# Kernel tuning notes

Measured on AMD Instinct MI355X. Metric: run time of the kernel, lower is better.

## Reference

```python
import jax, jax.numpy as jnp
import numpy as np

EPS = 1e-5

def conv1x1(x, w):
    # x: [B,C,H,W], w: [O,C] -> [B,O,H,W]
    return jnp.einsum('oc,bchw->bohw', w, x)

def bn(x, g, b, m, v):
    # inference batchnorm over channel dim 1
    scale = g / jnp.sqrt(v + EPS)
    return x * scale[None, :, None, None] + (b - m * scale)[None, :, None, None]

def setup_inputs() -> dict:
    key = jax.random.key(0)
    ks = jax.random.split(key, 20)
    B, Cin, S = 32, 256, 32
    C = Cin // 2
    rn = lambda k, sh: jax.random.normal(k, sh, dtype=jnp.float32)
    ru = lambda k, sh: jax.random.uniform(k, sh, dtype=jnp.float32)
    return {
        'x': rn(ks[0], (B, Cin, S, S)),
        'w1': rn(ks[1], (C, Cin)) * 0.05,
        'bn1_g': ru(ks[2], (C,)) + 0.5,
        'bn1_b': rn(ks[3], (C,)) * 0.1,
        'bn1_m': rn(ks[4], (C,)) * 0.1,
        'bn1_v': ru(ks[5], (C,)) + 0.5,
        'wq': rn(ks[6], (C, C)) * 0.05,
        'bq': rn(ks[7], (C,)) * 0.05,
        'wk': rn(ks[8], (C, C)) * 0.05,
        'bk': rn(ks[9], (C,)) * 0.05,
        'wv': rn(ks[10], (C, C)) * 0.05,
        'bv': rn(ks[11], (C,)) * 0.05,
        'rel_h': rn(ks[12], (1, C, S, 1)),
        'rel_w': rn(ks[13], (1, C, 1, S)),
        'w2': rn(ks[14], (Cin, C)) * 0.05,
        'bn2_g': ru(ks[15], (Cin,)) + 0.5,
        'bn2_b': rn(ks[16], (Cin,)) * 0.1,
        'bn2_m': rn(ks[17], (Cin,)) * 0.1,
        'bn2_v': ru(ks[18], (Cin,)) + 0.5,
    }

def reference(x, w1, bn1_g, bn1_b, bn1_m, bn1_v, wq, bq, wk, bk, wv, bv,
              rel_h, rel_w, w2, bn2_g, bn2_b, bn2_m, bn2_v):
    # cv1: 1x1 conv -> BN -> SiLU
    x1 = jax.nn.silu(bn(conv1x1(x, w1), bn1_g, bn1_b, bn1_m, bn1_v))
    B, C, H, W = x1.shape
    N = H * W
    # q/k/v: 1x1 conv with bias, flattened to [B,C,N]
    q = (conv1x1(x1, wq) + bq[None, :, None, None]).reshape(B, C, N)
    k = (conv1x1(x1, wk) + bk[None, :, None, None]).reshape(B, C, N)
    v = (conv1x1(x1, wv) + bv[None, :, None, None]).reshape(B, C, N)
    # content-content: q^T k -> [B,N,N]
    content_content = jnp.einsum('bci,bcj->bij', q, k)
    # content-position: pos^T q -> [B,N,N]
    pos = (rel_h + rel_w).reshape(C, N)  # [C,N]
    content_position = jnp.einsum('ci,bcj->bij', pos, q)
    attention = jax.nn.softmax(content_content + content_position, axis=-1)
    # out[b,c,i] = sum_j v[b,c,j] * attention[b,i,j]
    out = jnp.einsum('bcj,bij->bci', v, attention).reshape(B, C, H, W)
    # cv2: 1x1 conv -> BN -> SiLU, plus residual shortcut
    y = jax.nn.silu(bn(conv1x1(out, w2), bn2_g, bn2_b, bn2_m, bn2_v))
    return x + y
```

## Files before the change

### kernel.cpp

```cpp
#include <hip/hip_runtime.h>
#include <stdint.h>

typedef __bf16 bf16x8 __attribute__((ext_vector_type(8)));
typedef float  f32x4  __attribute__((ext_vector_type(4)));
typedef float  f32x16 __attribute__((ext_vector_type(16)));

#define MFMA(a,b,c)   __builtin_amdgcn_mfma_f32_16x16x32_bf16((a),(b),(c),0,0,0)
#define MFMA32(a,b,c) __builtin_amdgcn_mfma_f32_32x32x16_bf16((a),(b),(c),0,0,0)

__device__ __forceinline__ short f2b(float x) {
  uint32_t u = __float_as_uint(x);
  uint32_t r = (u + 0x7fffu + ((u >> 16) & 1u)) >> 16;
  return (short)r;
}

__device__ __forceinline__ uint32_t cvtpk(float lo, float hi) {
  uint32_t w;
  asm("v_cvt_pk_bf16_f32 %0, %1, %2" : "=v"(w) : "v"(lo), "v"(hi));
  return w;
}

__device__ __forceinline__ void glds16(const void* g, void* l) {
  __builtin_amdgcn_global_load_lds(
      (const __attribute__((address_space(1))) void*)(uintptr_t)g,
      (__attribute__((address_space(3))) void*)(uintptr_t)l, 16, 0, 0);
}

__global__ void k_prep(const float* __restrict__ w1, const float* __restrict__ wq,
                       const float* __restrict__ wk, const float* __restrict__ wv,
                       const float* __restrict__ w2,
                       const float* __restrict__ relh, const float* __restrict__ relw,
                       const float* __restrict__ g1, const float* __restrict__ b1,
                       const float* __restrict__ m1, const float* __restrict__ v1,
                       const float* __restrict__ g2, const float* __restrict__ b2,
                       const float* __restrict__ m2, const float* __restrict__ v2,
                       short* __restrict__ w1b, short* __restrict__ wqb,
                       short* __restrict__ wkb, short* __restrict__ wvb,
                       short* __restrict__ w2b, short* __restrict__ rhT,
                       short* __restrict__ rwT, float* __restrict__ bnc) {
  int i = blockIdx.x * 256 + threadIdx.x;
  if (i < 32768) { w1b[i] = f2b(w1[i]); return; }
  i -= 32768;
  if (i < 16384) { wqb[i] = f2b(wq[i]); return; }
  i -= 16384;
  if (i < 16384) { wkb[i] = f2b(wk[i]); return; }
  i -= 16384;
  if (i < 16384) { wvb[i] = f2b(wv[i]); return; }
  i -= 16384;
  if (i < 32768) { w2b[i] = f2b(w2[i]); return; }
  i -= 32768;
  if (i < 4096) { int h = i >> 7, c = i & 127; rhT[i] = f2b(relh[c * 32 + h]); return; }
  i -= 4096;
  if (i < 4096) { int w = i >> 7, c = i & 127; rwT[i] = f2b(relw[c * 32 + w]); return; }
  i -= 4096;
  if (i < 128) { float s = g1[i] * rsqrtf(v1[i] + 1e-5f); bnc[i] = s; bnc[128 + i] = b1[i] - m1[i] * s; return; }
  i -= 128;
  if (i < 256) { float s = g2[i] * rsqrtf(v2[i] + 1e-5f); bnc[256 + i] = s; bnc[512 + i] = b2[i] - m2[i] * s; return; }
}

__launch_bounds__(256)
__global__ void k_cq(const float* __restrict__ x, const short* __restrict__ w1b,
                     const short* __restrict__ wqb, const short* __restrict__ wkb,
                     const short* __restrict__ wvb, const float* __restrict__ bnc,
                     const float* __restrict__ bq, const float* __restrict__ bk,
                     const float* __restrict__ bv,
                     const short* __restrict__ rhT, const short* __restrict__ rwT,
                     short* __restrict__ qT, short* __restrict__ kT,
                     short* __restrict__ vv, float* __restrict__ Ug,
                     float* __restrict__ Wg) {
  __shared__ __align__(16) short Al[128 * 40];
  __shared__ __align__(16) short Bl[64 * 40];
  __shared__ __align__(16) short X1[64 * 136];
  const int bx = blockIdx.x;
  const int b = bx >> 4;
  const int n0 = (bx & 15) << 6;
  const int tid = threadIdx.x;
  const int wid = tid >> 6, lane = tid & 63;
  const int wr = wid >> 1, wc = wid & 1;
  const int cpr = lane & 15, g = lane >> 4;
  const int rl = lane & 31, hi2 = lane >> 5;
  const float* xb = x + (size_t)b * (256 * 1024);

  {
    f32x4 acc[4][2] = {};
    for (int kk = 0; kk < 8; ++kk) {
#pragma unroll
      for (int it = 0; it < 2; ++it) {
        int f = tid + it * 256;
        int row = f >> 2, c8 = f & 3;
        *reinterpret_cast<uint4*>(&Al[row * 40 + c8 * 8]) =
            *reinterpret_cast<const uint4*>(&w1b[row * 256 + kk * 32 + c8 * 8]);
      }
#pragma unroll
      for (int it = 0; it < 2; ++it) {
        int f = tid + it * 256;
        int ci = f >> 4, c4 = f & 15;
        float4 v4 = *reinterpret_cast<const float4*>(&xb[(size_t)(kk * 32 + ci) * 1024 + n0 + c4 * 4]);
        int nb = c4 * 4;
        Bl[(nb + 0) * 40 + ci] = f2b(v4.x);
        Bl[(nb + 1) * 40 + ci] = f2b(v4.y);
        Bl[(nb + 2) * 40 + ci] = f2b(v4.z);
        Bl[(nb + 3) * 40 + ci] = f2b(v4.w);
      }
      __syncthreads();
      bf16x8 af[4], bfr[2];
#pragma unroll
      for (int mf = 0; mf < 4; ++mf)
        af[mf] = *reinterpret_cast<const bf16x8*>(&Al[(wr * 64 + mf * 16 + cpr) * 40 + g * 8]);
#pragma unroll
      for (int nf = 0; nf < 2; ++nf)
        bfr[nf] = *reinterpret_cast<const bf16x8*>(&Bl[(wc * 32 + nf * 16 + cpr) * 40 + g * 8]);
#pragma unroll
      for (int mf = 0; mf < 4; ++mf)
#pragma unroll
        for (int nf = 0; nf < 2; ++nf)
          acc[mf][nf] = MFMA(af[mf], bfr[nf], acc[mf][nf]);
      __syncthreads();
    }
#pragma unroll
    for (int mf = 0; mf < 4; ++mf) {
      int m0 = wr * 64 + mf * 16 + g * 4;
#pragma unroll
      for (int nf = 0; nf < 2; ++nf) {
        int nl = wc * 32 + nf * 16 + cpr;
        union { short s[4]; uint2 u; } pk;
#pragma unroll
        for (int r = 0; r < 4; ++r) {
          int c = m0 + r;
          float z = acc[mf][nf][r] * bnc[c] + bnc[128 + c];
          pk.s[r] = f2b(z / (1.f + __expf(-z)));
        }
        *reinterpret_cast<uint2*>(&X1[nl * 136 + m0]) = pk.u;
      }
    }
  }
  __syncthreads();

  for (int which = 0; which < 3; ++which) {
    const short* W = which == 0 ? wvb : which == 1 ? wkb : wqb;
    const float* bias = which == 0 ? bv : which == 1 ? bk : bq;
    f32x4 acc[4][2] = {};
    for (int kk = 0; kk < 4; ++kk) {
#pragma unroll
      for (int it = 0; it < 2; ++it) {
        int f = tid + it * 256;
        int row = f >> 2, c8 = f & 3;
        *reinterpret_cast<uint4*>(&Al[row * 40 + c8 * 8]) =
            *reinterpret_cast<const uint4*>(&W[row * 128 + kk * 32 + c8 * 8]);
      }
      __syncthreads();
      bf16x8 af[4], bfr[2];
#pragma unroll
      for (int mf = 0; mf < 4; ++mf)
        af[mf] = *reinterpret_cast<const bf16x8*>(&Al[(wr * 64 + mf * 16 + cpr) * 40 + g * 8]);
#pragma unroll
      for (int nf = 0; nf < 2; ++nf)
        bfr[nf] = *reinterpret_cast<const bf16x8*>(&X1[(wc * 32 + nf * 16 + cpr) * 136 + kk * 32 + g * 8]);
#pragma unroll
      for (int mf = 0; mf < 4; ++mf)
#pragma unroll
        for (int nf = 0; nf < 2; ++nf)
          acc[mf][nf] = MFMA(af[mf], bfr[nf], acc[mf][nf]);
      __syncthreads();
    }
#pragma unroll
    for (int mf = 0; mf < 4; ++mf) {
      int m0 = wr * 64 + mf * 16 + g * 4;
#pragma unroll
      for (int nf = 0; nf < 2; ++nf) {
        int n = n0 + wc * 32 + nf * 16 + cpr;
        int nl = wc * 32 + nf * 16 + cpr;
        if (which == 0) {
#pragma unroll
          for (int r = 0; r < 4; ++r) {
            int c = m0 + r;
            vv[((size_t)b * 128 + c) * 1024 + n] = f2b(acc[mf][nf][r] + bias[c]);
          }
        } else {
          union { short s4[4]; uint2 u; } pk;
#pragma unroll
          for (int r = 0; r < 4; ++r)
            pk.s4[r] = f2b(acc[mf][nf][r] + bias[m0 + r]);
          if (which == 1) {
            *reinterpret_cast<uint2*>(&kT[((size_t)b * 1024 + n) * 128 + m0]) = pk.u;
          } else {
            *reinterpret_cast<uint2*>(&qT[((size_t)b * 1024 + n) * 128 + m0]) = pk.u;
            *reinterpret_cast<uint2*>(&X1[nl * 136 + m0]) = pk.u;
          }
        }
      }
    }
  }
  __syncthreads();

  {
    const int sel = wid >> 1, nh = wid & 1;
    const short* R = sel ? rwT : rhT;
    float* Og = sel ? Wg : Ug;
    f32x16 d = {};
#pragma unroll
    for (int ks = 0; ks < 8; ++ks) {
      bf16x8 aq = *reinterpret_cast<const bf16x8*>(&X1[(nh * 32 + rl) * 136 + ks * 16 + hi2 * 8]);
      bf16x8 br = *reinterpret_cast<const bf16x8*>(&R[(size_t)rl * 128 + ks * 16 + hi2 * 8]);
      d = MFMA32(aq, br, d);
    }
#pragma unroll
    for (int q2 = 0; q2 < 4; ++q2) {
      f32x4 v4 = { d[4 * q2 + 0], d[4 * q2 + 1], d[4 * q2 + 2], d[4 * q2 + 3] };
      *reinterpret_cast<f32x4*>(&Og[((size_t)b * 32 + rl) * 1024 + n0 + nh * 32 + q2 * 8 + hi2 * 4]) = v4;
    }
  }
}

__launch_bounds__(512, 1)
__global__ void k_attn(const short* __restrict__ qT, const short* __restrict__ kT,
                       const short* __restrict__ vv, const float* __restrict__ Ug,
                       const float* __restrict__ Wg,
                       const short* __restrict__ w2b, const float* __restrict__ bnc,
                       const float* __restrict__ x, float* __restrict__ out) {
  __shared__ __align__(16) char smem[100864];
  short* KhB0 = (short*)smem;
  short* KhB1 = (short*)(smem + 16384);
  short* VtB0 = (short*)(smem + 32768);
  short* VtB1 = (short*)(smem + 49152);
  float*    Obuf  = (float*)smem;
  uint16_t* ObufB = (uint16_t*)(smem + 66048);
  float*    mlf   = (float*)(smem + 98816);

  const int bx0 = blockIdx.x;
  const int lbx = ((bx0 & 7) << 5) | (bx0 >> 3);
  const int b  = lbx >> 3;
  const int i0 = (lbx & 7) << 7;
  const int tid = threadIdx.x;
  const int wid = tid >> 6, lane = tid & 63;
  const int rl = lane & 31, hi = lane >> 5;
  const int jh = wid >> 2, iq = wid & 3;
  const size_t bN = (size_t)b * 1024;
  const int hI = ((lbx & 7) << 2) + iq;

  const short* srcK[2];
  const short* srcV[2];
#pragma unroll
  for (int it = 0; it < 2; ++it) {
    int gq = it * 512 + tid;
    int row = gq >> 4, p = gq & 15;
    int l = p ^ (row & 7);
    srcK[it] = &kT[(bN + row) * 128 + l * 8];
  }
#pragma unroll
  for (int it = 0; it < 2; ++it) {
    int gq = it * 512 + tid;
    int c = gq >> 3, p = gq & 7;
    int l = p ^ (c & 7);
    srcV[it] = &vv[((size_t)b * 128 + c) * 1024 + l * 8];
  }
#pragma unroll
  for (int it = 0; it < 2; ++it) glds16(srcK[it], &KhB0[(it * 512 + wid * 64) * 8]);
#pragma unroll
  for (int it = 0; it < 2; ++it) glds16(srcV[it], &VtB0[(it * 512 + wid * 64) * 8]);

  bf16x8 qf[8];
  {
    const int irow = i0 + iq * 32 + rl;
#pragma unroll
    for (int ks = 0; ks < 8; ++ks)
      qf[ks] = *reinterpret_cast<const bf16x8*>(&qT[(bN + irow) * 128 + ks * 16 + hi * 8]);
  }
  __syncthreads();

  f32x16 oacc[4] = {};
  float mrow = -3e38f, lrow = 0.f;
  const float* Urow = &Ug[((size_t)b * 32 + hI) * 1024 + (jh << 5) + (hi << 2)];
  const float* Wrow = &Wg[((size_t)b * 32 + rl) * 1024 + (jh << 5) + (hi << 2)];

  for (int jt = 0; jt < 16; ++jt) {
    const int cur = jt & 1;
    f32x4 u4[4], w4[4];
#pragma unroll
    for (int g2 = 0; g2 < 4; ++g2) {
      u4[g2] = *reinterpret_cast<const f32x4*>(&Urow[(jt << 6) + g2 * 8]);
      w4[g2] = *reinterpret_cast<const f32x4*>(&Wrow[(jt << 6) + g2 * 8]);
    }
    if (jt < 15) {
      short* KhN = cur ? KhB0 : KhB1;
      short* VtN = cur ? VtB0 : VtB1;
#pragma unroll
      for (int it = 0; it < 2; ++it)
        glds16(srcK[it] + ((jt + 1) << 13), &KhN[(it * 512 + wid * 64) * 8]);
#pragma unroll
      for (int it = 0; it < 2; ++it)
        glds16(srcV[it] + ((jt + 1) << 6), &VtN[(it * 512 + wid * 64) * 8]);
    }
    const short* KhC = cur ? KhB1 : KhB0;
    const short* VtC = cur ? VtB1 : VtB0;

    f32x16 s0 = {}, s1 = {};
    {
      const int rb = (jh * 32 + rl) * 128;
      __builtin_amdgcn_s_setprio(1);
#pragma unroll
      for (int ks = 0; ks < 8; ++ks) {
        int p = ((ks << 1) | hi) ^ (rl & 7);
        bf16x8 kf = *reinterpret_cast<const bf16x8*>(&KhC[rb + p * 8]);
        if (ks & 1) s1 = MFMA32(kf, qf[ks], s1);
        else        s0 = MFMA32(kf, qf[ks], s0);
      }
      __builtin_amdgcn_s_setprio(0);
    }
    float t[16];
#pragma unroll
    for (int r = 0; r < 16; ++r)
      t[r] = s0[r] + s1[r] + u4[r >> 2][r & 3] + w4[r >> 2][r & 3];
    float mx = t[0];
#pragma unroll
    for (int r = 1; r < 16; ++r) mx = fmaxf(mx, t[r]);
    mx = fmaxf(mx, __shfl_xor(mx, 32));
    float pr[16];
    float ps = 0.f;
    if (__all(mx <= mrow + 8.f)) {
#pragma unroll
      for (int r = 0; r < 16; ++r) { pr[r] = __expf(t[r] - mrow); ps += pr[r]; }
      ps += __shfl_xor(ps, 32);
      lrow += ps;
    } else {
      float mnew = fmaxf(mrow, mx);
      float sc = __expf(mrow - mnew);
#pragma unroll
      for (int r = 0; r < 16; ++r) { pr[r] = __expf(t[r] - mnew); ps += pr[r]; }
      ps += __shfl_xor(ps, 32);
      lrow = lrow * sc + ps;
      mrow = mnew;
#pragma unroll
      for (int ct = 0; ct < 4; ++ct)
#pragma unroll
        for (int r = 0; r < 16; ++r) oacc[ct][r] *= sc;
    }
    uint32_t own[8], rcv[8];
#pragma unroll
    for (int idx = 0; idx < 8; ++idx) own[idx] = cvtpk(pr[2 * idx], pr[2 * idx + 1]);
#pragma unroll
    for (int idx = 0; idx < 8; ++idx) rcv[idx] = __shfl_xor((int)own[idx], 32);
#pragma unroll
    for (int js = 0; js < 2; ++js) {
      union { uint32_t u[4]; bf16x8 v; } pa;
      pa.u[0] = hi ? rcv[4 * js + 2] : own[4 * js + 0];
      pa.u[1] = hi ? rcv[4 * js + 3] : own[4 * js + 1];
      pa.u[2] = hi ? own[4 * js + 2] : rcv[4 * js + 0];
      pa.u[3] = hi ? own[4 * js + 3] : rcv[4 * js + 1];
      __builtin_amdgcn_s_setprio(1);
#pragma unroll
      for (int ct = 0; ct < 4; ++ct) {
        int c = ct * 32 + rl;
        int p = ((jh << 2) | (js << 1) | hi) ^ (rl & 7);
        bf16x8 vf = *reinterpret_cast<const bf16x8*>(&VtC[c * 64 + p * 8]);
        oacc[ct] = MFMA32(vf, pa.v, oacc[ct]);
      }
      __builtin_amdgcn_s_setprio(0);
    }
    __syncthreads();
  }

  if (lane < 32) {
    mlf[wid * 64 + rl]      = mrow;
    mlf[wid * 64 + 32 + rl] = lrow;
  }
  __syncthreads();
  float scl;
  {
    const int pid = wid ^ 4;
    float mp = mlf[pid * 64 + rl];
    float lp = mlf[pid * 64 + 32 + rl];
    float M  = fmaxf(mrow, mp);
    float f  = __expf(mrow - M);
    float fp = __expf(mp - M);
    scl = f / (lrow * f + lp * fp);
  }
  bf16x8 af2[8];
#pragma unroll
  for (int ks = 0; ks < 8; ++ks)
    af2[ks] = *reinterpret_cast<const bf16x8*>(&w2b[(size_t)(wid * 32 + rl) * 128 + ks * 16 + hi * 8]);
  __syncthreads();

  const int row = iq * 32 + rl;
  if (jh == 0) {
#pragma unroll
    for (int ct = 0; ct < 4; ++ct)
#pragma unroll
      for (int r = 0; r < 16; ++r) {
        int c = ct * 32 + (r & 3) + 8 * (r >> 2) + 4 * hi;
        Obuf[row * 129 + c] = oacc[ct][r] * scl;
      }
  }
  __syncthreads();
  if (jh == 1) {
    uint32_t* OW = (uint32_t*)ObufB;
#pragma unroll
    for (int ct = 0; ct < 4; ++ct) {
      float mg[16];
#pragma unroll
      for (int r = 0; r < 16; ++r) {
        int c = ct * 32 + (r & 3) + 8 * (r >> 2) + 4 * hi;
        mg[r] = Obuf[row * 129 + c] + oacc[ct][r] * scl;
      }
#pragma unroll
      for (int m = 0; m < 8; ++m) {
        int c0 = ct * 32 + ((2 * m) & 3) + 8 * ((2 * m) >> 2) + 4 * hi;
        int gI = c0 >> 3, wo = (c0 & 7) >> 1;
        int gS = gI ^ (row & 15);
        OW[row * 64 + gS * 4 + wo] = cvtpk(mg[2 * m], mg[2 * m + 1]);
      }
    }
  }
  __syncthreads();

  f32x16 a2[4] = {};
#pragma unroll
  for (int it = 0; it < 4; ++it) {
    const int r2 = it * 32 + rl;
    __builtin_amdgcn_s_setprio(1);
#pragma unroll
    for (int ks = 0; ks < 8; ++ks) {
      int gS = ((ks << 1) | hi) ^ (r2 & 15);
      bf16x8 bf = *reinterpret_cast<const bf16x8*>(&ObufB[r2 * 128 + gS * 8]);
      a2[it] = MFMA32(af2[ks], bf, a2[it]);
    }
    __builtin_amdgcn_s_setprio(0);
  }
  float bsc[16], bsh[16];
#pragma unroll
  for (int r = 0; r < 16; ++r) {
    int co = wid * 32 + (r & 3) + 8 * (r >> 2) + 4 * hi;
    bsc[r] = bnc[256 + co];
    bsh[r] = bnc[512 + co];
  }
#pragma unroll
  for (int it = 0; it < 4; ++it) {
#pragma unroll
    for (int r = 0; r < 16; ++r) {
      int co = wid * 32 + (r & 3) + 8 * (r >> 2) + 4 * hi;
      size_t idx = ((size_t)b * 256 + co) * 1024 + i0 + it * 32 + rl;
      float y = a2[it][r] * bsc[r] + bsh[r];
      out[idx] = x[idx] + y / (1.f + __expf(-y));
    }
  }
}

extern "C" void kernel_launch(void* const* d_in, const int* in_sizes, int n_in,
                              void* d_out, int out_size, void* d_ws, size_t ws_size,
                              hipStream_t stream) {
  (void)in_sizes; (void)n_in; (void)out_size; (void)ws_size;
  const float* x    = (const float*)d_in[0];
  const float* w1   = (const float*)d_in[1];
  const float* g1   = (const float*)d_in[2];
  const float* b1   = (const float*)d_in[3];
  const float* m1   = (const float*)d_in[4];
  const float* v1   = (const float*)d_in[5];
  const float* wq   = (const float*)d_in[6];
  const float* bq   = (const float*)d_in[7];
  const float* wk   = (const float*)d_in[8];
  const float* bk   = (const float*)d_in[9];
  const float* wv   = (const float*)d_in[10];
  const float* bv   = (const float*)d_in[11];
  const float* relh = (const float*)d_in[12];
  const float* relw = (const float*)d_in[13];
  const float* w2   = (const float*)d_in[14];
  const float* g2   = (const float*)d_in[15];
  const float* b2   = (const float*)d_in[16];
  const float* m2   = (const float*)d_in[17];
  const float* v2   = (const float*)d_in[18];
  float* out = (float*)d_out;

  char* ws = (char*)d_ws;
  const size_t OFF_W1B  = 0;
  const size_t OFF_WQB  = 65536;
  const size_t OFF_WKB  = 98304;
  const size_t OFF_WVB  = 131072;
  const size_t OFF_W2B  = 163840;
  const size_t OFF_RHT  = 229376;
  const size_t OFF_RWT  = 237568;
  const size_t OFF_BN   = 491520;
  const size_t OFF_QT   = 494592;
  const size_t OFF_KT   = OFF_QT + 8388608;
  const size_t OFF_V    = OFF_KT + 8388608;
  const size_t OFF_UG   = OFF_V + 8388608;
  const size_t OFF_WG   = OFF_UG + 4194304;

  short* w1b  = (short*)(ws + OFF_W1B);
  short* wqb  = (short*)(ws + OFF_WQB);
  short* wkb  = (short*)(ws + OFF_WKB);
  short* wvb  = (short*)(ws + OFF_WVB);
  short* w2b  = (short*)(ws + OFF_W2B);
  short* rhT  = (short*)(ws + OFF_RHT);
  short* rwT  = (short*)(ws + OFF_RWT);
  float* bnc  = (float*)(ws + OFF_BN);
  short* qT   = (short*)(ws + OFF_QT);
  short* kT   = (short*)(ws + OFF_KT);
  short* vv   = (short*)(ws + OFF_V);
  float* Ug   = (float*)(ws + OFF_UG);
  float* Wg   = (float*)(ws + OFF_WG);

  k_prep<<<482, 256, 0, stream>>>(w1, wq, wk, wv, w2, relh, relw,
                                  g1, b1, m1, v1, g2, b2, m2, v2,
                                  w1b, wqb, wkb, wvb, w2b, rhT, rwT, bnc);
  k_cq<<<512, 256, 0, stream>>>(x, w1b, wqb, wkb, wvb, bnc, bq, bk, bv,
                                rhT, rwT, qT, kT, vv, Ug, Wg);
  k_attn<<<256, 512, 0, stream>>>(qT, kT, vv, Ug, Wg, w2b, bnc, x, out);
}
```

Measured before the change: 90.82 us.

## Halve attention block to 64 query rows with 256 threads, two blocks per CU

The attention kernel now uses 512 blocks of 256 threads, each covering 64 query rows instead of 128, and shared memory shrinks so two blocks can share a CU. The split-KV merge no longer stages fp32 partials through LDS. Each half writes its scaled bf16 partial to its own buffer, and the output projection sums both through extra MFMAs. This is meant to raise occupancy and fill more CUs, and to remove a sync plus an fp32 LDS round trip. In exchange each block reloads the full K/V tiles, doubling K/V traffic per query row, and the partials are rounded to bf16 before they are summed.

```diff
diff --git a/kernel.cpp b/kernel.cpp
--- a/kernel.cpp
+++ b/kernel.cpp
@@ -212,52 +212,52 @@
   }
 }
 
-__launch_bounds__(512, 1)
+__launch_bounds__(256, 2)
 __global__ void k_attn(const short* __restrict__ qT, const short* __restrict__ kT,
                        const short* __restrict__ vv, const float* __restrict__ Ug,
                        const float* __restrict__ Wg,
                        const short* __restrict__ w2b, const float* __restrict__ bnc,
                        const float* __restrict__ x, float* __restrict__ out) {
-  __shared__ __align__(16) char smem[100864];
+  __shared__ __align__(16) char smem[66560];
   short* KhB0 = (short*)smem;
   short* KhB1 = (short*)(smem + 16384);
   short* VtB0 = (short*)(smem + 32768);
   short* VtB1 = (short*)(smem + 49152);
-  float*    Obuf  = (float*)smem;
-  uint16_t* ObufB = (uint16_t*)(smem + 66048);
-  float*    mlf   = (float*)(smem + 98816);
+  uint16_t* ObufB0 = (uint16_t*)smem;
+  uint16_t* ObufB1 = (uint16_t*)(smem + 16384);
+  float*    mlf    = (float*)(smem + 32768);
 
   const int bx0 = blockIdx.x;
-  const int lbx = ((bx0 & 7) << 5) | (bx0 >> 3);
-  const int b  = lbx >> 3;
-  const int i0 = (lbx & 7) << 7;
+  const int lbx = ((bx0 & 7) << 6) | (bx0 >> 3);
+  const int b  = lbx >> 4;
+  const int i0 = (lbx & 15) << 6;
   const int tid = threadIdx.x;
   const int wid = tid >> 6, lane = tid & 63;
   const int rl = lane & 31, hi = lane >> 5;
-  const int jh = wid >> 2, iq = wid & 3;
+  const int jh = wid >> 1, iq = wid & 1;
   const size_t bN = (size_t)b * 1024;
-  const int hI = ((lbx & 7) << 2) + iq;
-
-  const short* srcK[2];
-  const short* srcV[2];
-#pragma unroll
-  for (int it = 0; it < 2; ++it) {
-    int gq = it * 512 + tid;
+  const int hI = ((lbx & 15) << 1) + iq;
+
+  const short* srcK[4];
+  const short* srcV[4];
+#pragma unroll
+  for (int it = 0; it < 4; ++it) {
+    int gq = it * 256 + tid;
     int row = gq >> 4, p = gq & 15;
     int l = p ^ (row & 7);
     srcK[it] = &kT[(bN + row) * 128 + l * 8];
   }
 #pragma unroll
-  for (int it = 0; it < 2; ++it) {
-    int gq = it * 512 + tid;
+  for (int it = 0; it < 4; ++it) {
+    int gq = it * 256 + tid;
     int c = gq >> 3, p = gq & 7;
     int l = p ^ (c & 7);
     srcV[it] = &vv[((size_t)b * 128 + c) * 1024 + l * 8];
   }
 #pragma unroll
-  for (int it = 0; it < 2; ++it) glds16(srcK[it], &KhB0[(it * 512 + wid * 64) * 8]);
-#pragma unroll
-  for (int it = 0; it < 2; ++it) glds16(srcV[it], &VtB0[(it * 512 + wid * 64) * 8]);
+  for (int it = 0; it < 4; ++it) glds16(srcK[it], &KhB0[(it * 256 + wid * 64) * 8]);
+#pragma unroll
+  for (int it = 0; it < 4; ++it) glds16(srcV[it], &VtB0[(it * 256 + wid * 64) * 8]);
 
   bf16x8 qf[8];
   {
@@ -285,11 +285,11 @@
       short* KhN = cur ? KhB0 : KhB1;
       short* VtN = cur ? VtB0 : VtB1;
 #pragma unroll
-      for (int it = 0; it < 2; ++it)
-        glds16(srcK[it] + ((jt + 1) << 13), &KhN[(it * 512 + wid * 64) * 8]);
-#pragma unroll
-      for (int it = 0; it < 2; ++it)
-        glds16(srcV[it] + ((jt + 1) << 6), &VtN[(it * 512 + wid * 64) * 8]);
+      for (int it = 0; it < 4; ++it)
+        glds16(srcK[it] + ((jt + 1) << 13), &KhN[(it * 256 + wid * 64) * 8]);
+#pragma unroll
+      for (int it = 0; it < 4; ++it)
+        glds16(srcV[it] + ((jt + 1) << 6), &VtN[(it * 256 + wid * 64) * 8]);
     }
     const short* KhC = cur ? KhB1 : KhB0;
     const short* VtC = cur ? VtB1 : VtB0;
@@ -367,7 +367,7 @@
   __syncthreads();
   float scl;
   {
-    const int pid = wid ^ 4;
+    const int pid = wid ^ 2;
     float mp = mlf[pid * 64 + rl];
     float lp = mlf[pid * 64 + 32 + rl];
     float M  = fmaxf(mrow, mp);
@@ -375,72 +375,66 @@
     float fp = __expf(mp - M);
     scl = f / (lrow * f + lp * fp);
   }
-  bf16x8 af2[8];
-#pragma unroll
-  for (int ks = 0; ks < 8; ++ks)
-    af2[ks] = *reinterpret_cast<const bf16x8*>(&w2b[(size_t)(wid * 32 + rl) * 128 + ks * 16 + hi * 8]);
+  bf16x8 af2[2][8];
+#pragma unroll
+  for (int sub = 0; sub < 2; ++sub)
+#pragma unroll
+    for (int ks = 0; ks < 8; ++ks)
+      af2[sub][ks] = *reinterpret_cast<const bf16x8*>(
+          &w2b[(size_t)(wid * 64 + sub * 32 + rl) * 128 + ks * 16 + hi * 8]);
   __syncthreads();
 
-  const int row = iq * 32 + rl;
-  if (jh == 0) {
-#pragma unroll
-    for (int ct = 0; ct < 4; ++ct)
-#pragma unroll
-      for (int r = 0; r < 16; ++r) {
-        int c = ct * 32 + (r & 3) + 8 * (r >> 2) + 4 * hi;
-        Obuf[row * 129 + c] = oacc[ct][r] * scl;
-      }
-  }
-  __syncthreads();
-  if (jh == 1) {
-    uint32_t* OW = (uint32_t*)ObufB;
+  {
+    uint32_t* OW = (uint32_t*)(jh ? ObufB1 : ObufB0);
+    const int row = iq * 32 + rl;
 #pragma unroll
     for (int ct = 0; ct < 4; ++ct) {
-      float mg[16];
-#pragma unroll
-      for (int r = 0; r < 16; ++r) {
-        int c = ct * 32 + (r & 3) + 8 * (r >> 2) + 4 * hi;
-        mg[r] = Obuf[row * 129 + c] + oacc[ct][r] * scl;
-      }
 #pragma unroll
       for (int m = 0; m < 8; ++m) {
         int c0 = ct * 32 + ((2 * m) & 3) + 8 * ((2 * m) >> 2) + 4 * hi;
         int gI = c0 >> 3, wo = (c0 & 7) >> 1;
         int gS = gI ^ (row & 15);
-        OW[row * 64 + gS * 4 + wo] = cvtpk(mg[2 * m], mg[2 * m + 1]);
+        OW[row * 64 + gS * 4 + wo] = cvtpk(oacc[ct][2 * m] * scl, oacc[ct][2 * m + 1] * scl);
       }
     }
   }
   __syncthreads();
 
-  f32x16 a2[4] = {};
-#pragma unroll
-  for (int it = 0; it < 4; ++it) {
+  f32x16 a2[2][2] = {};
+#pragma unroll
+  for (int it = 0; it < 2; ++it) {
     const int r2 = it * 32 + rl;
     __builtin_amdgcn_s_setprio(1);
 #pragma unroll
     for (int ks = 0; ks < 8; ++ks) {
       int gS = ((ks << 1) | hi) ^ (r2 & 15);
-      bf16x8 bf = *reinterpret_cast<const bf16x8*>(&ObufB[r2 * 128 + gS * 8]);
-      a2[it] = MFMA32(af2[ks], bf, a2[it]);
+      bf16x8 bf0 = *reinterpret_cast<const bf16x8*>(&ObufB0[r2 * 128 + gS * 8]);
+      bf16x8 bf1 = *reinterpret_cast<const bf16x8*>(&ObufB1[r2 * 128 + gS * 8]);
+      a2[0][it] = MFMA32(af2[0][ks], bf0, a2[0][it]);
+      a2[1][it] = MFMA32(af2[1][ks], bf0, a2[1][it]);
+      a2[0][it] = MFMA32(af2[0][ks], bf1, a2[0][it]);
+      a2[1][it] = MFMA32(af2[1][ks], bf1, a2[1][it]);
     }
     __builtin_amdgcn_s_setprio(0);
   }
-  float bsc[16], bsh[16];
-#pragma unroll
-  for (int r = 0; r < 16; ++r) {
-    int co = wid * 32 + (r & 3) + 8 * (r >> 2) + 4 * hi;
-    bsc[r] = bnc[256 + co];
-    bsh[r] = bnc[512 + co];
-  }
-#pragma unroll
-  for (int it = 0; it < 4; ++it) {
+#pragma unroll
+  for (int sub = 0; sub < 2; ++sub) {
+    float bsc[16], bsh[16];
 #pragma unroll
     for (int r = 0; r < 16; ++r) {
-      int co = wid * 32 + (r & 3) + 8 * (r >> 2) + 4 * hi;
-      size_t idx = ((size_t)b * 256 + co) * 1024 + i0 + it * 32 + rl;
-      float y = a2[it][r] * bsc[r] + bsh[r];
-      out[idx] = x[idx] + y / (1.f + __expf(-y));
+      int co = wid * 64 + sub * 32 + (r & 3) + 8 * (r >> 2) + 4 * hi;
+      bsc[r] = bnc[256 + co];
+      bsh[r] = bnc[512 + co];
+    }
+#pragma unroll
+    for (int it = 0; it < 2; ++it) {
+#pragma unroll
+      for (int r = 0; r < 16; ++r) {
+        int co = wid * 64 + sub * 32 + (r & 3) + 8 * (r >> 2) + 4 * hi;
+        size_t idx = ((size_t)b * 256 + co) * 1024 + i0 + it * 32 + rl;
+        float y = a2[sub][it][r] * bsc[r] + bsh[r];
+        out[idx] = x[idx] + y / (1.f + __expf(-y));
+      }
     }
   }
 }
@@ -504,5 +498,5 @@
                                   w1b, wqb, wkb, wvb, w2b, rhT, rwT, bnc);
   k_cq<<<512, 256, 0, stream>>>(x, w1b, wqb, wkb, wvb, bnc, bq, bk, bv,
                                 rhT, rwT, qT, kT, vv, Ug, Wg);
-  k_attn<<<256, 512, 0, stream>>>(qT, kT, vv, Ug, Wg, w2b, bnc, x, out);
-}
+  k_attn<<<512, 256, 0, stream>>>(qT, kT, vv, Ug, Wg, w2b, bnc, x, out);
+}
```

Result: faster. 86.55 us (-4.7%).
